# Kernel optimization log

Measured on AMD Instinct MI355X. Metric: run time of the kernel, lower is better.

## Reference

```python
import jax, jax.numpy as jnp
import numpy as np

B, S, T = 4, 1024, 1024
CTX, QIN, C, H = 1024, 1024, 1024, 16
HD = C // H  # per-head channels


def setup_inputs() -> dict:
    key = jax.random.key(0)
    ks = jax.random.split(key, 12)
    s = 0.02
    return {
        "query": jax.random.normal(ks[0], (B, S, QIN), jnp.float32),
        "key": jax.random.normal(ks[1], (B, T, CTX), jnp.float32),
        "value": jax.random.normal(ks[2], (B, T, CTX), jnp.float32),
        "mask": jax.random.randint(ks[3], (B, S, T), 0, 2).astype(bool),
        "Wq": jax.random.normal(ks[4], (C, QIN), jnp.float32) * s,
        "bq": jax.random.normal(ks[5], (C,), jnp.float32) * s,
        "Wk": jax.random.normal(ks[6], (C, CTX), jnp.float32) * s,
        "bk": jax.random.normal(ks[7], (C,), jnp.float32) * s,
        "Wv": jax.random.normal(ks[8], (C, CTX), jnp.float32) * s,
        "bv": jax.random.normal(ks[9], (C,), jnp.float32) * s,
        "Wo": jax.random.normal(ks[10], (C, C), jnp.float32) * s,
        "bo": jax.random.normal(ks[11], (C,), jnp.float32) * s,
    }


def reference(query, key, value, mask, Wq, bq, Wk, bk, Wv, bv, Wo, bo):
    b, s, _ = query.shape
    t = key.shape[1]
    c = Wq.shape[0]
    h, hd = H, c // H
    q = (query @ Wq.T + bq).reshape(b, s, h, hd)
    k = (key @ Wk.T + bk).reshape(b, t, h, hd)
    v = (value @ Wv.T + bv).reshape(b, t, h, hd)
    # [B,H,S,T] scores, scaled by 1/sqrt(head_dim)
    score = jnp.einsum('bshd,bthd->bhst', q, k) * (hd ** -0.5)
    # masked_fill_(~mask[:, None, 0:1], -inf): mask key positions via row 0
    score = jnp.where(mask[:, None, 0:1], score, -jnp.inf)
    weights = jax.nn.softmax(score, axis=-1)
    out = jnp.einsum('bhst,bthd->bshd', weights, v).reshape(b, s, c)
    out = out @ Wo.T + bo
    out = out * mask[..., 0:1].astype(out.dtype)
    return out
```

## Files before the change

### kernel.cpp

```cpp
#include <hip/hip_runtime.h>
#include <stdint.h>

#define Bb  4
#define Ss  1024
#define Tt  1024
#define Cc  1024
#define Hh  16
#define HDd 64
#define Kk  1024

typedef __bf16 bf16;
typedef __bf16 bf16x8 __attribute__((ext_vector_type(8)));
typedef float  f32x4  __attribute__((ext_vector_type(4)));
typedef __attribute__((address_space(1))) uint32_t gu32;
typedef __attribute__((address_space(3))) uint32_t lu32;

__device__ __forceinline__ void load_lds16(const bf16* g, bf16* l) {
    __builtin_amdgcn_global_load_lds((gu32*)g, (lu32*)l, 16, 0, 0);
}

__global__ void cvt8(const float* __restrict__ s0, const float* __restrict__ s1,
                     const float* __restrict__ s2, const float* __restrict__ s3,
                     const float* __restrict__ s4, const float* __restrict__ s5,
                     const float* __restrict__ s6,
                     bf16* __restrict__ d0, bf16* __restrict__ d1,
                     bf16* __restrict__ d2, bf16* __restrict__ d3,
                     bf16* __restrict__ d4, bf16* __restrict__ d5,
                     bf16* __restrict__ d6)
{
    const float* s; bf16* d; int n;
    switch (blockIdx.y) {
        case 0: s = s0; d = d0; n = Bb * Ss * Kk; break;
        case 1: s = s1; d = d1; n = Bb * Ss * Kk; break;
        case 2: s = s2; d = d2; n = Bb * Ss * Kk; break;
        case 3: s = s3; d = d3; n = Cc * Kk; break;
        case 4: s = s4; d = d4; n = Cc * Kk; break;
        case 5: s = s5; d = d5; n = Cc * Kk; break;
        default: s = s6; d = d6; n = Cc * Kk; break;
    }
    const int i = (blockIdx.x * blockDim.x + threadIdx.x) * 8;
    if (i >= n) return;
    const float4 a = *(const float4*)(s + i);
    const float4 c = *(const float4*)(s + i + 4);
    bf16x8 o;
    o[0] = (bf16)a.x; o[1] = (bf16)a.y; o[2] = (bf16)a.z; o[3] = (bf16)a.w;
    o[4] = (bf16)c.x; o[5] = (bf16)c.y; o[6] = (bf16)c.z; o[7] = (bf16)c.w;
    *(bf16x8*)(d + i) = o;
}

__device__ __forceinline__ void mainloop_128x64(
    const bf16* __restrict__ Ab, const bf16* __restrict__ Wb,
    bf16* As, bf16* Bs, f32x4 acc[4][2])
{
    const int tid  = threadIdx.x;
    const int wid  = tid >> 6;
    const int lane = tid & 63;
    const int l16  = lane & 15;
    const int quad = lane >> 4;
    const int wm   = wid >> 1;
    const int wn   = wid & 1;
    const int r8   = lane >> 3;
    const int ssw  = ((lane & 7) ^ r8) * 8;

    for (int k0 = 0; k0 < Kk; k0 += 64) {
#pragma unroll
        for (int p = 0; p < 4; p++) {
            const int rb = wid * 32 + p * 8;
            load_lds16(Ab + (size_t)(rb + r8) * Kk + k0 + ssw, As + rb * 64);
        }
#pragma unroll
        for (int p = 0; p < 2; p++) {
            const int rb = wid * 16 + p * 8;
            load_lds16(Wb + (size_t)(rb + r8) * Kk + k0 + ssw, Bs + rb * 64);
        }
        __syncthreads();
#pragma unroll
        for (int kh = 0; kh < 2; kh++) {
            bf16x8 af[4], bw[2];
#pragma unroll
            for (int i = 0; i < 4; i++)
                af[i] = *(const bf16x8*)(As + (wm * 64 + i * 16 + l16) * 64 +
                                         (((kh * 4 + quad) ^ (l16 & 7)) * 8));
#pragma unroll
            for (int j = 0; j < 2; j++)
                bw[j] = *(const bf16x8*)(Bs + (wn * 32 + j * 16 + l16) * 64 +
                                         (((kh * 4 + quad) ^ (l16 & 7)) * 8));
#pragma unroll
            for (int i = 0; i < 4; i++)
#pragma unroll
                for (int j = 0; j < 2; j++)
                    acc[i][j] = __builtin_amdgcn_mfma_f32_16x16x32_bf16(af[i], bw[j], acc[i][j], 0, 0, 0);
        }
        __syncthreads();
    }
}

__device__ __forceinline__ void mainloop_64x64(
    const bf16* __restrict__ Ab, const bf16* __restrict__ Wb,
    bf16* As, bf16* Bs, f32x4 acc[2][2])
{
    const int tid  = threadIdx.x;
    const int wid  = tid >> 6;
    const int lane = tid & 63;
    const int l16  = lane & 15;
    const int quad = lane >> 4;
    const int wm   = wid >> 1;
    const int wn   = wid & 1;
    const int r8   = lane >> 3;
    const int ssw  = ((lane & 7) ^ r8) * 8;

    for (int k0 = 0; k0 < Kk; k0 += 64) {
#pragma unroll
        for (int p = 0; p < 2; p++) {
            const int rb = wid * 16 + p * 8;
            load_lds16(Ab + (size_t)(rb + r8) * Kk + k0 + ssw, As + rb * 64);
        }
#pragma unroll
        for (int p = 0; p < 2; p++) {
            const int rb = wid * 16 + p * 8;
            load_lds16(Wb + (size_t)(rb + r8) * Kk + k0 + ssw, Bs + rb * 64);
        }
        __syncthreads();
#pragma unroll
        for (int kh = 0; kh < 2; kh++) {
            bf16x8 af[2], bw[2];
#pragma unroll
            for (int i = 0; i < 2; i++)
                af[i] = *(const bf16x8*)(As + (wm * 32 + i * 16 + l16) * 64 +
                                         (((kh * 4 + quad) ^ (l16 & 7)) * 8));
#pragma unroll
            for (int j = 0; j < 2; j++)
                bw[j] = *(const bf16x8*)(Bs + (wn * 32 + j * 16 + l16) * 64 +
                                         (((kh * 4 + quad) ^ (l16 & 7)) * 8));
#pragma unroll
            for (int i = 0; i < 2; i++)
#pragma unroll
                for (int j = 0; j < 2; j++)
                    acc[i][j] = __builtin_amdgcn_mfma_f32_16x16x32_bf16(af[i], bw[j], acc[i][j], 0, 0, 0);
        }
        __syncthreads();
    }
}

__global__ __launch_bounds__(256)
void gemm_qkv(const bf16* __restrict__ Aq, const bf16* __restrict__ Ak, const bf16* __restrict__ Av,
              const bf16* __restrict__ Wq, const bf16* __restrict__ Wk, const bf16* __restrict__ Wv,
              const float* __restrict__ bq, const float* __restrict__ bk, const float* __restrict__ bv,
              bf16* __restrict__ Oq, bf16* __restrict__ Ok, bf16* __restrict__ Ov)
{
    __shared__ __align__(16) bf16 As[128 * 64];
    __shared__ __align__(16) bf16 Bs[64 * 64];
    const int z = blockIdx.z;
    const bf16*  A    = (z == 0) ? Aq : (z == 1) ? Ak : Av;
    const bf16*  W    = (z == 0) ? Wq : (z == 1) ? Wk : Wv;
    const float* bias = (z == 0) ? bq : (z == 1) ? bk : bv;
    bf16*        O    = (z == 0) ? Oq : (z == 1) ? Ok : Ov;

    f32x4 acc[4][2];
    const f32x4 z4 = {0.f, 0.f, 0.f, 0.f};
#pragma unroll
    for (int i = 0; i < 4; i++)
#pragma unroll
        for (int j = 0; j < 2; j++) acc[i][j] = z4;

    mainloop_128x64(A + (size_t)blockIdx.x * 128 * Kk,
                    W + (size_t)blockIdx.y * 64 * Kk, As, Bs, acc);

    const int tid = threadIdx.x;
    const int wid = tid >> 6, lane = tid & 63;
    const int l16 = lane & 15, quad = lane >> 4;
    const int wm = wid >> 1, wn = wid & 1;
    const int row0 = blockIdx.x * 128 + wm * 64;
    const int col0 = blockIdx.y * 64 + wn * 32;
#pragma unroll
    for (int j = 0; j < 2; j++) {
        const int col = col0 + j * 16 + l16;
        const float bj = bias[col];
        const int h = col >> 6, d = col & 63;
#pragma unroll
        for (int i = 0; i < 4; i++) {
#pragma unroll
            for (int r = 0; r < 4; r++) {
                const int row = row0 + i * 16 + quad * 4 + r;
                const int b = row >> 10, s = row & 1023;
                const bf16 val = (bf16)(acc[i][j][r] + bj);
                if (z == 2) {
                    Ov[((size_t)((b * Hh + h) * HDd + d)) * Tt + s] = val;
                } else {
                    O[((size_t)(b * Hh + h) * Ss + s) * HDd + d] = val;
                }
            }
        }
    }
}

__global__ __launch_bounds__(256)
void gemm_out(const bf16* __restrict__ A, const bf16* __restrict__ W,
              const float* __restrict__ bias, const int* __restrict__ mask,
              float* __restrict__ out)
{
    __shared__ __align__(16) bf16 As[64 * 64];
    __shared__ __align__(16) bf16 Bs[64 * 64];
    f32x4 acc[2][2];
    const f32x4 z4 = {0.f, 0.f, 0.f, 0.f};
#pragma unroll
    for (int i = 0; i < 2; i++)
#pragma unroll
        for (int j = 0; j < 2; j++) acc[i][j] = z4;

    mainloop_64x64(A + (size_t)blockIdx.x * 64 * Kk,
                   W + (size_t)blockIdx.y * 64 * Kk, As, Bs, acc);

    const int tid = threadIdx.x;
    const int wid = tid >> 6, lane = tid & 63;
    const int l16 = lane & 15, quad = lane >> 4;
    const int wm = wid >> 1, wn = wid & 1;
    const int row0 = blockIdx.x * 64 + wm * 32;
    const int col0 = blockIdx.y * 64 + wn * 32;
#pragma unroll
    for (int j = 0; j < 2; j++) {
        const int col = col0 + j * 16 + l16;
        const float bj = bias[col];
#pragma unroll
        for (int i = 0; i < 2; i++) {
#pragma unroll
            for (int r = 0; r < 4; r++) {
                const int row = row0 + i * 16 + quad * 4 + r;
                const float mval = (mask[(size_t)row * Tt] != 0) ? 1.f : 0.f;
                out[(size_t)row * Cc + col] = (acc[i][j][r] + bj) * mval;
            }
        }
    }
}

__global__ __launch_bounds__(256)
void attn(const bf16* __restrict__ Q, const bf16* __restrict__ Kp, const bf16* __restrict__ Vt,
          const int* __restrict__ mask, bf16* __restrict__ X)
{
    __shared__ __align__(16) bf16 Ks[64 * 64];
    __shared__ __align__(16) bf16 Vs[64 * 64];
    __shared__ __align__(16) bf16 Ps[4][16 * 72];
    const int g   = blockIdx.x;
    const int xcd = g & 7, idx = g >> 3;
    const int bh  = xcd * 8 + (idx >> 4);
    const int qblk = idx & 15;
    const int b = bh >> 4, h = bh & 15;
    const int tid = threadIdx.x, wid = tid >> 6, lane = tid & 63;
    const int l16 = lane & 15, quad = lane >> 4;
    const bf16* Qbh = Q  + (size_t)bh * Ss * HDd;
    const bf16* Kbh = Kp + (size_t)bh * Tt * HDd;
    const bf16* Vbh = Vt + (size_t)bh * HDd * Tt;
    const int*  mb  = mask + (size_t)b * Ss * Tt;
    const int q0 = qblk * 64 + wid * 16;
    bf16* Psw = &Ps[wid][0];

    const bf16x8 qf0 = *(const bf16x8*)(Qbh + (size_t)(q0 + l16) * HDd + quad * 8);
    const bf16x8 qf1 = *(const bf16x8*)(Qbh + (size_t)(q0 + l16) * HDd + 32 + quad * 8);

    float ls[4];
    f32x4 o[4];
    const f32x4 z4 = {0.f, 0.f, 0.f, 0.f};
#pragma unroll
    for (int r = 0; r < 4; r++) ls[r] = 0.f;
#pragma unroll
    for (int dblk = 0; dblk < 4; dblk++) o[dblk] = z4;

    const int srow = lane >> 3;
    const int schk = lane & 7;
    const int sswz = (schk ^ srow) * 8;

    for (int kt = 0; kt < Tt; kt += 64) {
#pragma unroll
        for (int p = 0; p < 2; p++) {
            const int c8 = wid * 2 + p;
            load_lds16(Kbh + (size_t)(kt + c8 * 8 + srow) * HDd + sswz,
                       Ks + c8 * 512);
            load_lds16(Vbh + (size_t)(c8 * 8 + srow) * Tt + kt + sswz,
                       Vs + c8 * 512);
        }
        __syncthreads();

        f32x4 sc[4];
#pragma unroll
        for (int nb = 0; nb < 4; nb++) sc[nb] = z4;
#pragma unroll
        for (int nb = 0; nb < 4; nb++) {
            const bf16* krow = Ks + (nb * 16 + l16) * 64;
            const bf16x8 kf0 = *(const bf16x8*)(krow + ((quad     ^ (l16 & 7)) * 8));
            const bf16x8 kf1 = *(const bf16x8*)(krow + (((4 + quad) ^ (l16 & 7)) * 8));
            sc[nb] = __builtin_amdgcn_mfma_f32_16x16x32_bf16(qf0, kf0, sc[nb], 0, 0, 0);
            sc[nb] = __builtin_amdgcn_mfma_f32_16x16x32_bf16(qf1, kf1, sc[nb], 0, 0, 0);
        }

#pragma unroll
        for (int nb = 0; nb < 4; nb++) {
            const float madd = mb[kt + nb * 16 + l16] ? 0.f : -1e30f;
#pragma unroll
            for (int r = 0; r < 4; r++) {
                const float p = __expf(sc[nb][r] * 0.125f + madd);
                ls[r] += p;
                Psw[(quad * 4 + r) * 72 + nb * 16 + l16] = (bf16)p;
            }
        }

#pragma unroll
        for (int kh = 0; kh < 2; kh++) {
            const bf16x8 pf = *(const bf16x8*)(Psw + l16 * 72 + kh * 32 + quad * 8);
#pragma unroll
            for (int dblk = 0; dblk < 4; dblk++) {
                const bf16x8 vf = *(const bf16x8*)(Vs + (dblk * 16 + l16) * 64 +
                                                   (((kh * 4 + quad) ^ (l16 & 7)) * 8));
                o[dblk] = __builtin_amdgcn_mfma_f32_16x16x32_bf16(pf, vf, o[dblk], 0, 0, 0);
            }
        }
        __syncthreads();
    }

#pragma unroll
    for (int off = 1; off <= 8; off <<= 1)
#pragma unroll
        for (int r = 0; r < 4; r++)
            ls[r] += __shfl_xor(ls[r], off, 64);
    float inv[4];
#pragma unroll
    for (int r = 0; r < 4; r++) inv[r] = 1.f / ls[r];

#pragma unroll
    for (int dblk = 0; dblk < 4; dblk++) {
#pragma unroll
        for (int r = 0; r < 4; r++) {
            const int srow_q = q0 + quad * 4 + r;
            const int d = dblk * 16 + l16;
            X[(size_t)(b * Ss + srow_q) * Cc + h * HDd + d] = (bf16)(o[dblk][r] * inv[r]);
        }
    }
}

extern "C" void kernel_launch(void* const* d_in, const int* in_sizes, int n_in,
                              void* d_out, int out_size, void* d_ws, size_t ws_size,
                              hipStream_t stream)
{
    const float* query = (const float*)d_in[0];
    const float* key   = (const float*)d_in[1];
    const float* value = (const float*)d_in[2];
    const int*   mask  = (const int*)d_in[3];
    const float* Wq = (const float*)d_in[4];
    const float* bq = (const float*)d_in[5];
    const float* Wk = (const float*)d_in[6];
    const float* bk = (const float*)d_in[7];
    const float* Wv = (const float*)d_in[8];
    const float* bv = (const float*)d_in[9];
    const float* Wo = (const float*)d_in[10];
    const float* bo = (const float*)d_in[11];
    float* out = (float*)d_out;

    char* ws = (char*)d_ws;
    const size_t MB = 1024 * 1024;
    bf16* qb  = (bf16*)(ws + 0 * MB);
    bf16* kb  = (bf16*)(ws + 8 * MB);
    bf16* vb  = (bf16*)(ws + 16 * MB);
    bf16* wqb = (bf16*)(ws + 24 * MB);
    bf16* wkb = (bf16*)(ws + 26 * MB);
    bf16* wvb = (bf16*)(ws + 28 * MB);
    bf16* wob = (bf16*)(ws + 30 * MB);
    bf16* Qp  = (bf16*)(ws + 32 * MB);
    bf16* Kpp = (bf16*)(ws + 40 * MB);
    bf16* Vtp = (bf16*)(ws + 48 * MB);
    bf16* Xb  = (bf16*)(ws + 56 * MB);

    cvt8<<<dim3(2048, 7), 256, 0, stream>>>(query, key, value, Wq, Wk, Wv, Wo,
                                            qb, kb, vb, wqb, wkb, wvb, wob);
    gemm_qkv<<<dim3(32, 16, 3), 256, 0, stream>>>(qb, kb, vb, wqb, wkb, wvb,
                                                  bq, bk, bv, Qp, Kpp, Vtp);
    attn<<<dim3(1024), 256, 0, stream>>>(Qp, Kpp, Vtp, mask, Xb);
    gemm_out<<<dim3(64, 16), 256, 0, stream>>>(Xb, wob, bo, mask, out);
}
```

Before: 232.9 us.

## Enlarge GEMM tiles and register-prefetch K/V tiles in attention loop

```diff
diff --git a/kernel.cpp b/kernel.cpp
--- a/kernel.cpp
+++ b/kernel.cpp
@@ -18,6 +18,11 @@
 __device__ __forceinline__ void load_lds16(const bf16* g, bf16* l) {
     __builtin_amdgcn_global_load_lds((gu32*)g, (lu32*)l, 16, 0, 0);
 }
+
+#define BARRIER_LDS() do {                                    \
+    asm volatile("s_waitcnt lgkmcnt(0)" ::: "memory");        \
+    __builtin_amdgcn_s_barrier();                             \
+} while (0)
 
 __global__ void cvt8(const float* __restrict__ s0, const float* __restrict__ s1,
                      const float* __restrict__ s2, const float* __restrict__ s3,
@@ -48,9 +53,10 @@
     *(bf16x8*)(d + i) = o;
 }
 
-__device__ __forceinline__ void mainloop_128x64(
+
+__device__ __forceinline__ void mainloop_128x128(
     const bf16* __restrict__ Ab, const bf16* __restrict__ Wb,
-    bf16* As, bf16* Bs, f32x4 acc[4][2])
+    bf16* As, bf16* Bs, f32x4 acc[4][4])
 {
     const int tid  = threadIdx.x;
     const int wid  = tid >> 6;
@@ -67,37 +73,33 @@
         for (int p = 0; p < 4; p++) {
             const int rb = wid * 32 + p * 8;
             load_lds16(Ab + (size_t)(rb + r8) * Kk + k0 + ssw, As + rb * 64);
-        }
-#pragma unroll
-        for (int p = 0; p < 2; p++) {
-            const int rb = wid * 16 + p * 8;
             load_lds16(Wb + (size_t)(rb + r8) * Kk + k0 + ssw, Bs + rb * 64);
         }
         __syncthreads();
 #pragma unroll
         for (int kh = 0; kh < 2; kh++) {
-            bf16x8 af[4], bw[2];
+            bf16x8 af[4], bw[4];
 #pragma unroll
             for (int i = 0; i < 4; i++)
                 af[i] = *(const bf16x8*)(As + (wm * 64 + i * 16 + l16) * 64 +
                                          (((kh * 4 + quad) ^ (l16 & 7)) * 8));
 #pragma unroll
-            for (int j = 0; j < 2; j++)
-                bw[j] = *(const bf16x8*)(Bs + (wn * 32 + j * 16 + l16) * 64 +
+            for (int j = 0; j < 4; j++)
+                bw[j] = *(const bf16x8*)(Bs + (wn * 64 + j * 16 + l16) * 64 +
                                          (((kh * 4 + quad) ^ (l16 & 7)) * 8));
 #pragma unroll
             for (int i = 0; i < 4; i++)
 #pragma unroll
-                for (int j = 0; j < 2; j++)
+                for (int j = 0; j < 4; j++)
                     acc[i][j] = __builtin_amdgcn_mfma_f32_16x16x32_bf16(af[i], bw[j], acc[i][j], 0, 0, 0);
         }
         __syncthreads();
     }
 }
 
-__device__ __forceinline__ void mainloop_64x64(
+__device__ __forceinline__ void mainloop_128x64(
     const bf16* __restrict__ Ab, const bf16* __restrict__ Wb,
-    bf16* As, bf16* Bs, f32x4 acc[2][2])
+    bf16* As, bf16* Bs, f32x4 acc[4][2])
 {
     const int tid  = threadIdx.x;
     const int wid  = tid >> 6;
@@ -111,8 +113,8 @@
 
     for (int k0 = 0; k0 < Kk; k0 += 64) {
 #pragma unroll
-        for (int p = 0; p < 2; p++) {
-            const int rb = wid * 16 + p * 8;
+        for (int p = 0; p < 4; p++) {
+            const int rb = wid * 32 + p * 8;
             load_lds16(Ab + (size_t)(rb + r8) * Kk + k0 + ssw, As + rb * 64);
         }
 #pragma unroll
@@ -123,17 +125,17 @@
         __syncthreads();
 #pragma unroll
         for (int kh = 0; kh < 2; kh++) {
-            bf16x8 af[2], bw[2];
-#pragma unroll
-            for (int i = 0; i < 2; i++)
-                af[i] = *(const bf16x8*)(As + (wm * 32 + i * 16 + l16) * 64 +
+            bf16x8 af[4], bw[2];
+#pragma unroll
+            for (int i = 0; i < 4; i++)
+                af[i] = *(const bf16x8*)(As + (wm * 64 + i * 16 + l16) * 64 +
                                          (((kh * 4 + quad) ^ (l16 & 7)) * 8));
 #pragma unroll
             for (int j = 0; j < 2; j++)
                 bw[j] = *(const bf16x8*)(Bs + (wn * 32 + j * 16 + l16) * 64 +
                                          (((kh * 4 + quad) ^ (l16 & 7)) * 8));
 #pragma unroll
-            for (int i = 0; i < 2; i++)
+            for (int i = 0; i < 4; i++)
 #pragma unroll
                 for (int j = 0; j < 2; j++)
                     acc[i][j] = __builtin_amdgcn_mfma_f32_16x16x32_bf16(af[i], bw[j], acc[i][j], 0, 0, 0);
@@ -149,31 +151,31 @@
               bf16* __restrict__ Oq, bf16* __restrict__ Ok, bf16* __restrict__ Ov)
 {
     __shared__ __align__(16) bf16 As[128 * 64];
-    __shared__ __align__(16) bf16 Bs[64 * 64];
+    __shared__ __align__(16) bf16 Bs[128 * 64];
     const int z = blockIdx.z;
     const bf16*  A    = (z == 0) ? Aq : (z == 1) ? Ak : Av;
     const bf16*  W    = (z == 0) ? Wq : (z == 1) ? Wk : Wv;
     const float* bias = (z == 0) ? bq : (z == 1) ? bk : bv;
     bf16*        O    = (z == 0) ? Oq : (z == 1) ? Ok : Ov;
 
-    f32x4 acc[4][2];
+    f32x4 acc[4][4];
     const f32x4 z4 = {0.f, 0.f, 0.f, 0.f};
 #pragma unroll
     for (int i = 0; i < 4; i++)
 #pragma unroll
-        for (int j = 0; j < 2; j++) acc[i][j] = z4;
-
-    mainloop_128x64(A + (size_t)blockIdx.x * 128 * Kk,
-                    W + (size_t)blockIdx.y * 64 * Kk, As, Bs, acc);
+        for (int j = 0; j < 4; j++) acc[i][j] = z4;
+
+    mainloop_128x128(A + (size_t)blockIdx.x * 128 * Kk,
+                     W + (size_t)blockIdx.y * 128 * Kk, As, Bs, acc);
 
     const int tid = threadIdx.x;
     const int wid = tid >> 6, lane = tid & 63;
     const int l16 = lane & 15, quad = lane >> 4;
     const int wm = wid >> 1, wn = wid & 1;
     const int row0 = blockIdx.x * 128 + wm * 64;
-    const int col0 = blockIdx.y * 64 + wn * 32;
-#pragma unroll
-    for (int j = 0; j < 2; j++) {
+    const int col0 = blockIdx.y * 128 + wn * 64;
+#pragma unroll
+    for (int j = 0; j < 4; j++) {
         const int col = col0 + j * 16 + l16;
         const float bj = bias[col];
         const int h = col >> 6, d = col & 63;
@@ -199,30 +201,30 @@
               const float* __restrict__ bias, const int* __restrict__ mask,
               float* __restrict__ out)
 {
-    __shared__ __align__(16) bf16 As[64 * 64];
+    __shared__ __align__(16) bf16 As[128 * 64];
     __shared__ __align__(16) bf16 Bs[64 * 64];
-    f32x4 acc[2][2];
+    f32x4 acc[4][2];
     const f32x4 z4 = {0.f, 0.f, 0.f, 0.f};
 #pragma unroll
-    for (int i = 0; i < 2; i++)
+    for (int i = 0; i < 4; i++)
 #pragma unroll
         for (int j = 0; j < 2; j++) acc[i][j] = z4;
 
-    mainloop_64x64(A + (size_t)blockIdx.x * 64 * Kk,
-                   W + (size_t)blockIdx.y * 64 * Kk, As, Bs, acc);
+    mainloop_128x64(A + (size_t)blockIdx.x * 128 * Kk,
+                    W + (size_t)blockIdx.y * 64 * Kk, As, Bs, acc);
 
     const int tid = threadIdx.x;
     const int wid = tid >> 6, lane = tid & 63;
     const int l16 = lane & 15, quad = lane >> 4;
     const int wm = wid >> 1, wn = wid & 1;
-    const int row0 = blockIdx.x * 64 + wm * 32;
+    const int row0 = blockIdx.x * 128 + wm * 64;
     const int col0 = blockIdx.y * 64 + wn * 32;
 #pragma unroll
     for (int j = 0; j < 2; j++) {
         const int col = col0 + j * 16 + l16;
         const float bj = bias[col];
 #pragma unroll
-        for (int i = 0; i < 2; i++) {
+        for (int i = 0; i < 4; i++) {
 #pragma unroll
             for (int r = 0; r < 4; r++) {
                 const int row = row0 + i * 16 + quad * 4 + r;
@@ -233,7 +235,7 @@
     }
 }
 
-__global__ __launch_bounds__(256)
+__global__ __launch_bounds__(256, 4)
 void attn(const bf16* __restrict__ Q, const bf16* __restrict__ Kp, const bf16* __restrict__ Vt,
           const int* __restrict__ mask, bf16* __restrict__ X)
 {
@@ -268,33 +270,59 @@
     const int srow = lane >> 3;
     const int schk = lane & 7;
     const int sswz = (schk ^ srow) * 8;
-
-    for (int kt = 0; kt < Tt; kt += 64) {
-#pragma unroll
-        for (int p = 0; p < 2; p++) {
-            const int c8 = wid * 2 + p;
-            load_lds16(Kbh + (size_t)(kt + c8 * 8 + srow) * HDd + sswz,
-                       Ks + c8 * 512);
-            load_lds16(Vbh + (size_t)(c8 * 8 + srow) * Tt + kt + sswz,
-                       Vs + c8 * 512);
-        }
-        __syncthreads();
-
+    const int c80 = wid * 2, c81 = wid * 2 + 1;
+
+    const bf16* kg0 = Kbh + (size_t)(c80 * 8 + srow) * HDd + sswz;
+    const bf16* kg1 = Kbh + (size_t)(c81 * 8 + srow) * HDd + sswz;
+    const bf16* vg0 = Vbh + (size_t)(c80 * 8 + srow) * Tt + sswz;
+    const bf16* vg1 = Vbh + (size_t)(c81 * 8 + srow) * Tt + sswz;
+    bf16* kd0 = Ks + c80 * 512 + lane * 8;
+    bf16* kd1 = Ks + c81 * 512 + lane * 8;
+    bf16* vd0 = Vs + c80 * 512 + lane * 8;
+    bf16* vd1 = Vs + c81 * 512 + lane * 8;
+
+    bf16x8 ka0, ka1, va0, va1;
+    bf16x8 kb0, kb1, vb0, vb1;
+    int mA0, mA1, mA2, mA3, mB0, mB1, mB2, mB3;
+
+#define LOADA(KT) do { const int _kt = (KT);                          \
+    ka0 = *(const bf16x8*)(kg0 + (size_t)_kt * HDd);                  \
+    ka1 = *(const bf16x8*)(kg1 + (size_t)_kt * HDd);                  \
+    va0 = *(const bf16x8*)(vg0 + _kt);                                \
+    va1 = *(const bf16x8*)(vg1 + _kt);                                \
+    mA0 = mb[_kt + l16];      mA1 = mb[_kt + 16 + l16];               \
+    mA2 = mb[_kt + 32 + l16]; mA3 = mb[_kt + 48 + l16]; } while (0)
+#define LOADB(KT) do { const int _kt = (KT);                          \
+    kb0 = *(const bf16x8*)(kg0 + (size_t)_kt * HDd);                  \
+    kb1 = *(const bf16x8*)(kg1 + (size_t)_kt * HDd);                  \
+    vb0 = *(const bf16x8*)(vg0 + _kt);                                \
+    vb1 = *(const bf16x8*)(vg1 + _kt);                                \
+    mB0 = mb[_kt + l16];      mB1 = mb[_kt + 16 + l16];               \
+    mB2 = mb[_kt + 32 + l16]; mB3 = mb[_kt + 48 + l16]; } while (0)
+#define STOREA() do {                                                 \
+    *(bf16x8*)kd0 = ka0; *(bf16x8*)kd1 = ka1;                         \
+    *(bf16x8*)vd0 = va0; *(bf16x8*)vd1 = va1; } while (0)
+#define STOREB() do {                                                 \
+    *(bf16x8*)kd0 = kb0; *(bf16x8*)kd1 = kb1;                         \
+    *(bf16x8*)vd0 = vb0; *(bf16x8*)vd1 = vb1; } while (0)
+
+    auto compute = [&](int m0, int m1, int m2, int m3) {
         f32x4 sc[4];
 #pragma unroll
         for (int nb = 0; nb < 4; nb++) sc[nb] = z4;
 #pragma unroll
         for (int nb = 0; nb < 4; nb++) {
             const bf16* krow = Ks + (nb * 16 + l16) * 64;
-            const bf16x8 kf0 = *(const bf16x8*)(krow + ((quad     ^ (l16 & 7)) * 8));
+            const bf16x8 kf0 = *(const bf16x8*)(krow + ((quad       ^ (l16 & 7)) * 8));
             const bf16x8 kf1 = *(const bf16x8*)(krow + (((4 + quad) ^ (l16 & 7)) * 8));
             sc[nb] = __builtin_amdgcn_mfma_f32_16x16x32_bf16(qf0, kf0, sc[nb], 0, 0, 0);
             sc[nb] = __builtin_amdgcn_mfma_f32_16x16x32_bf16(qf1, kf1, sc[nb], 0, 0, 0);
         }
 
+        const int mm[4] = {m0, m1, m2, m3};
 #pragma unroll
         for (int nb = 0; nb < 4; nb++) {
-            const float madd = mb[kt + nb * 16 + l16] ? 0.f : -1e30f;
+            const float madd = mm[nb] ? 0.f : -1e30f;
 #pragma unroll
             for (int r = 0; r < 4; r++) {
                 const float p = __expf(sc[nb][r] * 0.125f + madd);
@@ -313,8 +341,27 @@
                 o[dblk] = __builtin_amdgcn_mfma_f32_16x16x32_bf16(pf, vf, o[dblk], 0, 0, 0);
             }
         }
-        __syncthreads();
-    }
+    };
+
+    LOADA(0);
+
+    for (int kt = 0; kt < Tt; kt += 128) {
+        BARRIER_LDS();
+        LOADB(kt + 64);
+        STOREA();
+        BARRIER_LDS();
+        compute(mA0, mA1, mA2, mA3);
+
+        BARRIER_LDS();
+        LOADA((kt + 128 < Tt) ? (kt + 128) : (Tt - 64));
+        STOREB();
+        BARRIER_LDS();
+        compute(mB0, mB1, mB2, mB3);
+    }
+#undef LOADA
+#undef LOADB
+#undef STOREA
+#undef STOREB
 
 #pragma unroll
     for (int off = 1; off <= 8; off <<= 1)
@@ -370,8 +417,8 @@
 
     cvt8<<<dim3(2048, 7), 256, 0, stream>>>(query, key, value, Wq, Wk, Wv, Wo,
                                             qb, kb, vb, wqb, wkb, wvb, wob);
-    gemm_qkv<<<dim3(32, 16, 3), 256, 0, stream>>>(qb, kb, vb, wqb, wkb, wvb,
-                                                  bq, bk, bv, Qp, Kpp, Vtp);
+    gemm_qkv<<<dim3(32, 8, 3), 256, 0, stream>>>(qb, kb, vb, wqb, wkb, wvb,
+                                                 bq, bk, bv, Qp, Kpp, Vtp);
     attn<<<dim3(1024), 256, 0, stream>>>(Qp, Kpp, Vtp, mask, Xb);
-    gemm_out<<<dim3(64, 16), 256, 0, stream>>>(Xb, wob, bo, mask, out);
-}
+    gemm_out<<<dim3(32, 16), 256, 0, stream>>>(Xb, wob, bo, mask, out);
+}
```

Result: no change. 233.2 us (+0.1%).
